# Kernel tuning notes

Hardware: AMD Instinct MI355X
Metric: run time of the kernel (lower is better)

The kernel has to match this reference:

```python
import jax, jax.numpy as jnp
import numpy as np

B, N, D, H = 4, 2048, 512, 8
HD = D // H  # 64


def setup_inputs() -> dict:
    key = jax.random.key(0)
    ks = jax.random.split(key, 12)
    s = 0.02
    return {
        "x": jax.random.normal(ks[0], (B, N, D), jnp.float32),
        "freqs": jax.random.normal(ks[1], (B, N, HD // 2), jnp.float32),
        # weights stored as (in, out); torch Linear applies x @ W.T + b
        "wqkv_w": jax.random.normal(ks[2], (D, 3 * D), jnp.float32) * s,
        "wqkv_b": jax.random.normal(ks[3], (3 * D,), jnp.float32) * s,
        "out_w": jax.random.normal(ks[4], (D, D), jnp.float32) * s,
        "out_b": jax.random.normal(ks[5], (D,), jnp.float32) * s,
        "ffn1_w": jax.random.normal(ks[6], (2 * D, 2 * D), jnp.float32) * s,
        "ffn1_b": jax.random.normal(ks[7], (2 * D,), jnp.float32) * s,
        "ln_g": jnp.ones((2 * D,), jnp.float32),
        "ln_b": jnp.zeros((2 * D,), jnp.float32),
        "ffn2_w": jax.random.normal(ks[8], (2 * D, D), jnp.float32) * s,
        "ffn2_b": jax.random.normal(ks[9], (D,), jnp.float32) * s,
    }


def _rope(t, cos, sin):
    # t: [B,H,N,HD]; cos/sin: [B,1,N,HD/2]
    x1, x2 = t[..., ::2], t[..., 1::2]
    return jnp.stack([x1 * cos - x2 * sin, x1 * sin + x2 * cos], axis=-1).reshape(t.shape)


def reference(x, freqs, wqkv_w, wqkv_b, out_w, out_b,
              ffn1_w, ffn1_b, ln_g, ln_b, ffn2_w, ffn2_b):
    b, n, d = x.shape
    h, hd = H, d // H
    qkv = x @ wqkv_w + wqkv_b                      # [B,N,3D]
    q, k, v = jnp.split(qkv, 3, axis=-1)
    to_heads = lambda t: t.reshape(b, n, h, hd).transpose(0, 2, 1, 3)  # [B,H,N,HD]
    q, k, v = to_heads(q), to_heads(k), to_heads(v)
    cos = jnp.cos(freqs)[:, None]                  # [B,1,N,HD/2]
    sin = jnp.sin(freqs)[:, None]
    q = _rope(q, cos, sin)
    k = _rope(k, cos, sin)
    scale = hd ** -0.5
    attn = jax.nn.softmax(jnp.einsum('bhqd,bhkd->bhqk', q, k) * scale, axis=-1)
    msg = jnp.einsum('bhqk,bhkd->bhqd', attn, v).transpose(0, 2, 1, 3).reshape(b, n, d)
    msg = msg @ out_w + out_b
    # FFN on concat([x, msg]): Linear -> LayerNorm -> GELU(exact) -> Linear
    hcat = jnp.concatenate([x, msg], axis=-1) @ ffn1_w + ffn1_b   # [B,N,2D]
    mu = hcat.mean(-1, keepdims=True)
    var = hcat.var(-1, keepdims=True)
    hcat = (hcat - mu) * jax.lax.rsqrt(var + 1e-5) * ln_g + ln_b
    hcat = jax.nn.gelu(hcat, approximate=False)
    return x + hcat @ ffn2_w + ffn2_b
```

## Files before the change

### kernel.cpp

```cpp
#include <hip/hip_runtime.h>
#include <hip/hip_bf16.h>
#include <math.h>

typedef __bf16 bf16;
typedef __bf16 bf16x2 __attribute__((ext_vector_type(2)));
typedef __bf16 bf16x4 __attribute__((ext_vector_type(4)));
typedef __bf16 bf16x8 __attribute__((ext_vector_type(8)));
typedef float f32x4 __attribute__((ext_vector_type(4)));
typedef float f32x16 __attribute__((ext_vector_type(16)));

#define MFMA16(a, b, c) __builtin_amdgcn_mfma_f32_16x16x32_bf16(a, b, c, 0, 0, 0)
#define MFMA32(a, b, c) __builtin_amdgcn_mfma_f32_32x32x16_bf16(a, b, c, 0, 0, 0)

#define GLD_LDS16(gp, lp)                                                          \
    __builtin_amdgcn_global_load_lds(                                              \
        (const __attribute__((address_space(1))) void*)(gp),                       \
        (__attribute__((address_space(3))) void*)(lp), 16, 0, 0)


__global__ __launch_bounds__(256) void transpose_all_kernel(
    const float* __restrict__ w0, const float* __restrict__ w1,
    const float* __restrict__ w2, const float* __restrict__ w3,
    bf16* __restrict__ d0, bf16* __restrict__ d1,
    bf16* __restrict__ d2, bf16* __restrict__ d3)
{
    const int bid = blockIdx.x;
    const float* src; bf16* dst; int R, C, bx, by;
    if (bid < 768)       { src = w0; dst = d0; R = 512;  C = 1536; int r = bid;        bx = r % 48; by = r / 48; }
    else if (bid < 1024) { src = w1; dst = d1; R = 512;  C = 512;  int r = bid - 768;  bx = r % 16; by = r / 16; }
    else if (bid < 2048) { src = w2; dst = d2; R = 1024; C = 1024; int r = bid - 1024; bx = r % 32; by = r / 32; }
    else                 { src = w3; dst = d3; R = 1024; C = 512;  int r = bid - 2048; bx = r % 16; by = r / 16; }
    __shared__ bf16 tile[32][33];
    const int tx = threadIdx.x & 31, ty = threadIdx.x >> 5;
    const int x = bx * 32 + tx;
#pragma unroll
    for (int j = 0; j < 4; j++)
        tile[ty + 8 * j][tx] = (bf16)src[(size_t)(by * 32 + ty + 8 * j) * C + x];
    __syncthreads();
    const int x2 = by * 32 + tx;
#pragma unroll
    for (int j = 0; j < 4; j++)
        dst[(size_t)(bx * 32 + ty + 8 * j) * R + x2] = tile[tx][ty + 8 * j];
}

__global__ __launch_bounds__(256) void cast_x_kernel(const float* __restrict__ x,
                                                     bf16* __restrict__ cat)
{
    int i = blockIdx.x * 256 + threadIdx.x;
    int row = i >> 7, col = (i & 127) << 2;
    const float4 v = *(const float4*)(&x[(size_t)row * 512 + col]);
    bf16x4 o; o[0] = (bf16)v.x; o[1] = (bf16)v.y; o[2] = (bf16)v.z; o[3] = (bf16)v.w;
    *(bf16x4*)(&cat[(size_t)row * 1024 + col]) = o;
}

__global__ __launch_bounds__(256) void rope_kernel(bf16* __restrict__ qb,
                                                   bf16* __restrict__ kb,
                                                   const float* __restrict__ freqs)
{
    const float SC = 0.125f * 1.44269504089f;
    const int bh = blockIdx.x >> 6, nblk = blockIdx.x & 63;
    const int g = threadIdx.x & 7, nl = threadIdx.x >> 3;
    const int n = nblk * 32 + nl;
    const int b = bh >> 3;
    const float4 f = *(const float4*)(&freqs[((size_t)b * 2048 + n) * 32 + g * 4]);
    const float cs[4] = {cosf(f.x), cosf(f.y), cosf(f.z), cosf(f.w)};
    const float sn[4] = {sinf(f.x), sinf(f.y), sinf(f.z), sinf(f.w)};
    const size_t off = ((size_t)bh * 2048 + n) * 64 + g * 8;
    bf16x8 q8 = *(bf16x8*)(qb + off);
    bf16x8 k8 = *(bf16x8*)(kb + off);
#pragma unroll
    for (int i = 0; i < 4; i++) {
        float q1 = q8[2 * i], q2 = q8[2 * i + 1];
        q8[2 * i]     = (bf16)((q1 * cs[i] - q2 * sn[i]) * SC);
        q8[2 * i + 1] = (bf16)((q1 * sn[i] + q2 * cs[i]) * SC);
        float k1 = k8[2 * i], k2 = k8[2 * i + 1];
        k8[2 * i]     = (bf16)(k1 * cs[i] - k2 * sn[i]);
        k8[2 * i + 1] = (bf16)(k1 * sn[i] + k2 * cs[i]);
    }
    *(bf16x8*)(qb + off) = q8;
    *(bf16x8*)(kb + off) = k8;
}

template <int MODE>
__global__ __launch_bounds__(256) void gemm_mfma(
    const bf16* __restrict__ A, int lda, const bf16* __restrict__ Bt,
    const float* __restrict__ bias, void* __restrict__ outv,
    const float* __restrict__ auxf, bf16* __restrict__ o1, bf16* __restrict__ o2,
    int K)
{
    const int tid = threadIdx.x;
    const int lane = tid & 63;
    const int wave = tid >> 6;
    const int wm = wave >> 1, wn = wave & 1;
    const int l15 = lane & 15, quad = lane >> 4;
    const int m0 = blockIdx.y * 128;
    const int n0 = blockIdx.x * 128;

    __shared__ bf16 As[128 * 32];
    __shared__ bf16 Bs[128 * 32];

    const int c0 = tid, c1 = tid + 256;
    const int r0 = c0 >> 2, kc0 = (c0 & 3) << 3;
    const int r1 = c1 >> 2, kc1 = (c1 & 3) << 3;

    const f32x4 zero = {0.f, 0.f, 0.f, 0.f};
    f32x4 acc[4][4];
#pragma unroll
    for (int i = 0; i < 4; i++)
#pragma unroll
        for (int j = 0; j < 4; j++) acc[i][j] = zero;

    for (int k0 = 0; k0 < K; k0 += 32) {
        GLD_LDS16(&A[(size_t)(m0 + r0) * lda + k0 + kc0], &As[c0 * 8]);
        GLD_LDS16(&A[(size_t)(m0 + r1) * lda + k0 + kc1], &As[c1 * 8]);
        GLD_LDS16(&Bt[(size_t)(n0 + r0) * K + k0 + kc0], &Bs[c0 * 8]);
        GLD_LDS16(&Bt[(size_t)(n0 + r1) * K + k0 + kc1], &Bs[c1 * 8]);
        __syncthreads();
        bf16x8 af[4], bfv[4];
#pragma unroll
        for (int t = 0; t < 4; t++) {
            af[t]  = *(const bf16x8*)(&As[(wm * 64 + t * 16 + l15) * 32 + quad * 8]);
            bfv[t] = *(const bf16x8*)(&Bs[(wn * 64 + t * 16 + l15) * 32 + quad * 8]);
        }
#pragma unroll
        for (int mt = 0; mt < 4; mt++)
#pragma unroll
            for (int nt = 0; nt < 4; nt++)
                acc[mt][nt] = MFMA16(af[mt], bfv[nt], acc[mt][nt]);
        __syncthreads();
    }

    const int row_base = m0 + wm * 64;
    const int col_base = n0 + wn * 64;

    if constexpr (MODE == 0) {
        const int sector = col_base >> 9;
        bf16* dstbase = (sector == 0) ? (bf16*)outv : (sector == 1 ? o1 : o2);
#pragma unroll
        for (int nt = 0; nt < 4; nt++) {
            const int col = col_base + nt * 16 + l15;
            const int cq = col & 511;
            const int h = cq >> 6, hd = cq & 63;
            const float bv = bias[col];
#pragma unroll
            for (int mt = 0; mt < 4; mt++) {
#pragma unroll
                for (int r = 0; r < 4; r++) {
                    const int mrow = row_base + mt * 16 + quad * 4 + r;
                    const int b = mrow >> 11, n = mrow & 2047;
                    dstbase[(((size_t)b * 8 + h) * 2048 + n) * 64 + hd] =
                        (bf16)(acc[mt][nt][r] + bv);
                }
            }
        }
    } else {
#pragma unroll
        for (int nt = 0; nt < 4; nt++) {
            const int col = col_base + nt * 16 + l15;
            const float bv = bias[col];
#pragma unroll
            for (int mt = 0; mt < 4; mt++) {
#pragma unroll
                for (int r = 0; r < 4; r++) {
                    const int row = row_base + mt * 16 + quad * 4 + r;
                    float v = acc[mt][nt][r] + bv;
                    if constexpr (MODE == 1) {
                        ((bf16*)outv)[(size_t)row * 1024 + 512 + col] = (bf16)v;
                    } else if constexpr (MODE == 2) {
                        ((bf16*)outv)[(size_t)row * 1024 + col] = (bf16)v;
                    } else {
                        v += auxf[(size_t)row * 512 + col];
                        ((float*)outv)[(size_t)row * 512 + col] = v;
                    }
                }
            }
        }
    }
}

__global__ __launch_bounds__(256) void attn_kernel(const bf16* __restrict__ qb,
                                                   const bf16* __restrict__ kb,
                                                   const bf16* __restrict__ vb,
                                                   bf16* __restrict__ ao)
{
    __shared__ bf16 Ks[128 * 72];
    __shared__ bf16 Vts[64 * 136];
    __shared__ bf16 Ps[4][32 * 72];

    const int tid = threadIdx.x, lane = tid & 63, wave = tid >> 6;
    const int l31 = lane & 31, half = lane >> 5;
    const int bh = blockIdx.x >> 4, qt = blockIdx.x & 15;
    const int b = bh >> 3, h = bh & 7;
    const size_t base = (size_t)bh * 2048 * 64;
    const int m0 = qt * 128 + wave * 32;

    bf16x8 aq[4];
#pragma unroll
    for (int k4 = 0; k4 < 4; k4++)
        aq[k4] = *(const bf16x8*)(&qb[base + (size_t)(m0 + l31) * 64 + k4 * 16 + half * 8]);

    f32x16 accO[2];
    float lsum[16];
#pragma unroll
    for (int i = 0; i < 16; i++) { accO[0][i] = 0.f; accO[1][i] = 0.f; lsum[i] = 0.f; }

    int krow[4], kcol[4], vpr[2], vdg[2];
#pragma unroll
    for (int i = 0; i < 4; i++) { int c = tid + i * 256; krow[i] = c >> 3; kcol[i] = (c & 7) << 3; }
#pragma unroll
    for (int i = 0; i < 2; i++) { int t = tid + i * 256; vpr[i] = t & 63; vdg[i] = t >> 6; }

    bf16x8 kreg[4], vreg0[2], vreg1[2];
    auto prefetch = [&](int key0) {
#pragma unroll
        for (int i = 0; i < 4; i++)
            kreg[i] = *(const bf16x8*)(&kb[base + (size_t)(key0 + krow[i]) * 64 + kcol[i]]);
#pragma unroll
        for (int i = 0; i < 2; i++) {
            vreg0[i] = *(const bf16x8*)(&vb[base + (size_t)(key0 + 2 * vpr[i]) * 64 + vdg[i] * 8]);
            vreg1[i] = *(const bf16x8*)(&vb[base + (size_t)(key0 + 2 * vpr[i] + 1) * 64 + vdg[i] * 8]);
        }
    };

    prefetch(0);
    for (int kt = 0; kt < 16; kt++) {
        __syncthreads();
#pragma unroll
        for (int i = 0; i < 4; i++)
            *(bf16x8*)(&Ks[krow[i] * 72 + kcol[i]]) = kreg[i];
#pragma unroll
        for (int i = 0; i < 2; i++) {
#pragma unroll
            for (int j = 0; j < 8; j++) {
                bf16x2 pr; pr[0] = vreg0[i][j]; pr[1] = vreg1[i][j];
                *(bf16x2*)(&Vts[(vdg[i] * 8 + j) * 136 + 2 * vpr[i]]) = pr;
            }
        }
        __syncthreads();
        if (kt < 15) prefetch((kt + 1) * 128);

#pragma unroll
        for (int sub = 0; sub < 2; sub++) {
            const int ko = sub * 64;
#pragma unroll
            for (int nb = 0; nb < 2; nb++) {
                f32x16 s;
#pragma unroll
                for (int i = 0; i < 16; i++) s[i] = 0.f;
#pragma unroll
                for (int k4 = 0; k4 < 4; k4++) {
                    bf16x8 bk = *(const bf16x8*)(&Ks[(ko + nb * 32 + l31) * 72 + k4 * 16 + half * 8]);
                    s = MFMA32(aq[k4], bk, s);
                }
#pragma unroll
                for (int r = 0; r < 16; r++) {
                    float pv = exp2f(s[r]);
                    lsum[r] += pv;
                    const int rowq = (r & 3) + 8 * (r >> 2) + 4 * half;
                    Ps[wave][rowq * 72 + nb * 32 + l31] = (bf16)pv;
                }
            }
#pragma unroll
            for (int kh = 0; kh < 4; kh++) {
                bf16x8 ap = *(const bf16x8*)(&Ps[wave][l31 * 72 + kh * 16 + half * 8]);
#pragma unroll
                for (int nb2 = 0; nb2 < 2; nb2++) {
                    bf16x8 bv = *(const bf16x8*)(&Vts[(nb2 * 32 + l31) * 136 + ko + kh * 16 + half * 8]);
                    accO[nb2] = MFMA32(ap, bv, accO[nb2]);
                }
            }
        }
    }

    float inv[16];
#pragma unroll
    for (int r = 0; r < 16; r++) {
        float s = lsum[r];
        s += __shfl_xor(s, 1); s += __shfl_xor(s, 2);
        s += __shfl_xor(s, 4); s += __shfl_xor(s, 8); s += __shfl_xor(s, 16);
        inv[r] = 1.0f / s;
    }

#pragma unroll
    for (int nb = 0; nb < 2; nb++) {
#pragma unroll
        for (int r = 0; r < 16; r++) {
            const int n = m0 + (r & 3) + 8 * (r >> 2) + 4 * half;
            ao[((size_t)b * 2048 + n) * 512 + h * 64 + nb * 32 + l31] =
                (bf16)(accO[nb][r] * inv[r]);
        }
    }
}

__global__ __launch_bounds__(256) void ln_gelu_kernel(bf16* __restrict__ hb,
                                                      const float* __restrict__ g,
                                                      const float* __restrict__ bt)
{
    const int row = blockIdx.x, tid = threadIdx.x;
    const int lane = tid & 63, wave = tid >> 6;
    bf16* hr = hb + (size_t)row * 1024;
    bf16x4 hv = *(const bf16x4*)(&hr[tid * 4]);
    float v0 = hv[0], v1 = hv[1], v2 = hv[2], v3 = hv[3];
    float s = v0 + v1 + v2 + v3;
    float q = v0 * v0 + v1 * v1 + v2 * v2 + v3 * v3;
    for (int o = 32; o; o >>= 1) { s += __shfl_xor(s, o); q += __shfl_xor(q, o); }
    __shared__ float red[8];
    if (lane == 0) { red[wave] = s; red[4 + wave] = q; }
    __syncthreads();
    s = red[0] + red[1] + red[2] + red[3];
    q = red[4] + red[5] + red[6] + red[7];
    const float mu = s * (1.f / 1024.f);
    const float rstd = rsqrtf(q * (1.f / 1024.f) - mu * mu + 1e-5f);
    const float4 gv = *(const float4*)(&g[tid * 4]);
    const float4 bv = *(const float4*)(&bt[tid * 4]);
    float vv[4] = {v0, v1, v2, v3};
    const float gg[4] = {gv.x, gv.y, gv.z, gv.w};
    const float bb[4] = {bv.x, bv.y, bv.z, bv.w};
    bf16x4 o4;
#pragma unroll
    for (int i = 0; i < 4; i++) {
        float y = (vv[i] - mu) * rstd * gg[i] + bb[i];
        float ge = 0.5f * y * (1.0f + erff(y * 0.70710678118f));
        o4[i] = (bf16)ge;
    }
    *(bf16x4*)(&hr[tid * 4]) = o4;
}

extern "C" void kernel_launch(void* const* d_in, const int* in_sizes, int n_in,
                              void* d_out, int out_size, void* d_ws, size_t ws_size,
                              hipStream_t stream) {
    (void)in_sizes; (void)n_in; (void)out_size; (void)ws_size;
    const float* x      = (const float*)d_in[0];
    const float* freqs  = (const float*)d_in[1];
    const float* wqkv_w = (const float*)d_in[2];
    const float* wqkv_b = (const float*)d_in[3];
    const float* out_w  = (const float*)d_in[4];
    const float* out_b  = (const float*)d_in[5];
    const float* ffn1_w = (const float*)d_in[6];
    const float* ffn1_b = (const float*)d_in[7];
    const float* ln_g   = (const float*)d_in[8];
    const float* ln_b   = (const float*)d_in[9];
    const float* ffn2_w = (const float*)d_in[10];
    const float* ffn2_b = (const float*)d_in[11];
    float* out = (float*)d_out;
    bf16* ws   = (bf16*)d_ws;

    bf16* wqkv_t = ws;
    bf16* out_t  = wqkv_t + 1536 * 512;
    bf16* ffn1_t = out_t + 512 * 512;
    bf16* ffn2_t = ffn1_t + 1024 * 1024;
    bf16* cat    = ffn2_t + 512 * 1024;
    bf16* qbuf   = cat + (size_t)8192 * 1024;
    bf16* kbuf   = qbuf + (size_t)8192 * 512;
    bf16* vbuf   = kbuf + (size_t)8192 * 512;
    bf16* aobuf  = vbuf + (size_t)8192 * 512;
    bf16* hbuf   = qbuf;

    transpose_all_kernel<<<2560, 256, 0, stream>>>(wqkv_w, out_w, ffn1_w, ffn2_w,
                                                   wqkv_t, out_t, ffn1_t, ffn2_t);
    cast_x_kernel<<<4096, 256, 0, stream>>>(x, cat);

    gemm_mfma<0><<<dim3(12, 64), 256, 0, stream>>>(cat, 1024, wqkv_t, wqkv_b, qbuf, nullptr, kbuf, vbuf, 512);
    rope_kernel<<<2048, 256, 0, stream>>>(qbuf, kbuf, freqs);
    attn_kernel<<<512, 256, 0, stream>>>(qbuf, kbuf, vbuf, aobuf);
    gemm_mfma<1><<<dim3(4, 64), 256, 0, stream>>>(aobuf, 512, out_t, out_b, cat, nullptr, nullptr, nullptr, 512);
    gemm_mfma<2><<<dim3(8, 64), 256, 0, stream>>>(cat, 1024, ffn1_t, ffn1_b, hbuf, nullptr, nullptr, nullptr, 1024);
    ln_gelu_kernel<<<8192, 256, 0, stream>>>(hbuf, ln_g, ln_b);
    gemm_mfma<3><<<dim3(4, 64), 256, 0, stream>>>(hbuf, 1024, ffn2_t, ffn2_b, out, x, nullptr, nullptr, 1024);
}
```

Measured before the change: 293.5 us.

## Keep attention probabilities in registers via transposed MFMA and register-prefetch GEMM tiles

The attention kernel now computes the transposed score tile (K as the A operand, Q as the B operand), so each lane holds one query row's probabilities. Those are packed to bf16 and swapped across wave halves with shuffles to form the PV MFMA operand directly, removing the per-wave LDS staging buffer and its store/load round trip. This also simplifies row-sum reduction and allows vectorized output stores. Separately, the GEMM replaces direct global-to-LDS loads with a register prefetch of the next K-slice that overlaps the MFMA work, at the cost of extra VGPRs and explicit LDS writes.

```diff
diff --git a/kernel.cpp b/kernel.cpp
--- a/kernel.cpp
+++ b/kernel.cpp
@@ -11,11 +11,6 @@
 
 #define MFMA16(a, b, c) __builtin_amdgcn_mfma_f32_16x16x32_bf16(a, b, c, 0, 0, 0)
 #define MFMA32(a, b, c) __builtin_amdgcn_mfma_f32_32x32x16_bf16(a, b, c, 0, 0, 0)
-
-#define GLD_LDS16(gp, lp)                                                          \
-    __builtin_amdgcn_global_load_lds(                                              \
-        (const __attribute__((address_space(1))) void*)(gp),                       \
-        (__attribute__((address_space(3))) void*)(lp), 16, 0, 0)
 
 
 __global__ __launch_bounds__(256) void transpose_all_kernel(
@@ -103,6 +98,11 @@
     const int r0 = c0 >> 2, kc0 = (c0 & 3) << 3;
     const int r1 = c1 >> 2, kc1 = (c1 & 3) << 3;
 
+    const bf16* pA0 = &A[(size_t)(m0 + r0) * lda + kc0];
+    const bf16* pA1 = &A[(size_t)(m0 + r1) * lda + kc1];
+    const bf16* pB0 = &Bt[(size_t)(n0 + r0) * K + kc0];
+    const bf16* pB1 = &Bt[(size_t)(n0 + r1) * K + kc1];
+
     const f32x4 zero = {0.f, 0.f, 0.f, 0.f};
     f32x4 acc[4][4];
 #pragma unroll
@@ -110,12 +110,24 @@
 #pragma unroll
         for (int j = 0; j < 4; j++) acc[i][j] = zero;
 
+    bf16x8 ra0 = *(const bf16x8*)pA0;
+    bf16x8 ra1 = *(const bf16x8*)pA1;
+    bf16x8 rb0 = *(const bf16x8*)pB0;
+    bf16x8 rb1 = *(const bf16x8*)pB1;
+
     for (int k0 = 0; k0 < K; k0 += 32) {
-        GLD_LDS16(&A[(size_t)(m0 + r0) * lda + k0 + kc0], &As[c0 * 8]);
-        GLD_LDS16(&A[(size_t)(m0 + r1) * lda + k0 + kc1], &As[c1 * 8]);
-        GLD_LDS16(&Bt[(size_t)(n0 + r0) * K + k0 + kc0], &Bs[c0 * 8]);
-        GLD_LDS16(&Bt[(size_t)(n0 + r1) * K + k0 + kc1], &Bs[c1 * 8]);
         __syncthreads();
+        *(bf16x8*)(&As[c0 * 8]) = ra0;
+        *(bf16x8*)(&As[c1 * 8]) = ra1;
+        *(bf16x8*)(&Bs[c0 * 8]) = rb0;
+        *(bf16x8*)(&Bs[c1 * 8]) = rb1;
+        __syncthreads();
+        if (k0 + 32 < K) {
+            ra0 = *(const bf16x8*)(pA0 + k0 + 32);
+            ra1 = *(const bf16x8*)(pA1 + k0 + 32);
+            rb0 = *(const bf16x8*)(pB0 + k0 + 32);
+            rb1 = *(const bf16x8*)(pB1 + k0 + 32);
+        }
         bf16x8 af[4], bfv[4];
 #pragma unroll
         for (int t = 0; t < 4; t++) {
@@ -127,7 +139,6 @@
 #pragma unroll
             for (int nt = 0; nt < 4; nt++)
                 acc[mt][nt] = MFMA16(af[mt], bfv[nt], acc[mt][nt]);
-        __syncthreads();
     }
 
     const int row_base = m0 + wm * 64;
@@ -185,7 +196,6 @@
 {
     __shared__ bf16 Ks[128 * 72];
     __shared__ bf16 Vts[64 * 136];
-    __shared__ bf16 Ps[4][32 * 72];
 
     const int tid = threadIdx.x, lane = tid & 63, wave = tid >> 6;
     const int l31 = lane & 31, half = lane >> 5;
@@ -200,9 +210,9 @@
         aq[k4] = *(const bf16x8*)(&qb[base + (size_t)(m0 + l31) * 64 + k4 * 16 + half * 8]);
 
     f32x16 accO[2];
-    float lsum[16];
-#pragma unroll
-    for (int i = 0; i < 16; i++) { accO[0][i] = 0.f; accO[1][i] = 0.f; lsum[i] = 0.f; }
+#pragma unroll
+    for (int i = 0; i < 16; i++) { accO[0][i] = 0.f; accO[1][i] = 0.f; }
+    float lsum = 0.f;
 
     int krow[4], kcol[4], vpr[2], vdg[2];
 #pragma unroll
@@ -240,54 +250,68 @@
         if (kt < 15) prefetch((kt + 1) * 128);
 
 #pragma unroll
-        for (int sub = 0; sub < 2; sub++) {
-            const int ko = sub * 64;
-#pragma unroll
-            for (int nb = 0; nb < 2; nb++) {
-                f32x16 s;
-#pragma unroll
-                for (int i = 0; i < 16; i++) s[i] = 0.f;
-#pragma unroll
-                for (int k4 = 0; k4 < 4; k4++) {
-                    bf16x8 bk = *(const bf16x8*)(&Ks[(ko + nb * 32 + l31) * 72 + k4 * 16 + half * 8]);
-                    s = MFMA32(aq[k4], bk, s);
-                }
-#pragma unroll
-                for (int r = 0; r < 16; r++) {
-                    float pv = exp2f(s[r]);
-                    lsum[r] += pv;
-                    const int rowq = (r & 3) + 8 * (r >> 2) + 4 * half;
-                    Ps[wave][rowq * 72 + nb * 32 + l31] = (bf16)pv;
-                }
-            }
-#pragma unroll
-            for (int kh = 0; kh < 4; kh++) {
-                bf16x8 ap = *(const bf16x8*)(&Ps[wave][l31 * 72 + kh * 16 + half * 8]);
-#pragma unroll
-                for (int nb2 = 0; nb2 < 2; nb2++) {
-                    bf16x8 bv = *(const bf16x8*)(&Vts[(nb2 * 32 + l31) * 136 + ko + kh * 16 + half * 8]);
-                    accO[nb2] = MFMA32(ap, bv, accO[nb2]);
-                }
-            }
-        }
-    }
-
-    float inv[16];
-#pragma unroll
-    for (int r = 0; r < 16; r++) {
-        float s = lsum[r];
-        s += __shfl_xor(s, 1); s += __shfl_xor(s, 2);
-        s += __shfl_xor(s, 4); s += __shfl_xor(s, 8); s += __shfl_xor(s, 16);
-        inv[r] = 1.0f / s;
-    }
-
-#pragma unroll
-    for (int nb = 0; nb < 2; nb++) {
-#pragma unroll
-        for (int r = 0; r < 16; r++) {
-            const int n = m0 + (r & 3) + 8 * (r >> 2) + 4 * half;
-            ao[((size_t)b * 2048 + n) * 512 + h * 64 + nb * 32 + l31] =
-                (bf16)(accO[nb][r] * inv[r]);
+        for (int nb = 0; nb < 4; nb++) {
+            const int ko = nb * 32;
+            f32x16 s;
+#pragma unroll
+            for (int i = 0; i < 16; i++) s[i] = 0.f;
+#pragma unroll
+            for (int k4 = 0; k4 < 4; k4++) {
+                bf16x8 ak = *(const bf16x8*)(&Ks[(ko + l31) * 72 + k4 * 16 + half * 8]);
+                s = MFMA32(ak, aq[k4], s);
+            }
+            float p[16];
+#pragma unroll
+            for (int r = 0; r < 16; r++) p[r] = exp2f(s[r]);
+            lsum += (((p[0] + p[1]) + (p[2] + p[3])) + ((p[4] + p[5]) + (p[6] + p[7])))
+                  + (((p[8] + p[9]) + (p[10] + p[11])) + ((p[12] + p[13]) + (p[14] + p[15])));
+            unsigned pk[8];
+#pragma unroll
+            for (int i2 = 0; i2 < 8; i2++) {
+                union { bf16x2 hh; unsigned u; } t;
+                t.hh[0] = (bf16)p[2 * i2]; t.hh[1] = (bf16)p[2 * i2 + 1];
+                pk[i2] = t.u;
+            }
+            const unsigned sa = half ? pk[0] : pk[2];
+            const unsigned sb = half ? pk[1] : pk[3];
+            const unsigned sc2 = half ? pk[4] : pk[6];
+            const unsigned sd = half ? pk[5] : pk[7];
+            const unsigned ra = (unsigned)__shfl_xor((int)sa, 32);
+            const unsigned rb = (unsigned)__shfl_xor((int)sb, 32);
+            const unsigned rc = (unsigned)__shfl_xor((int)sc2, 32);
+            const unsigned rd = (unsigned)__shfl_xor((int)sd, 32);
+            union { bf16x8 v; unsigned u[4]; } B0, B1;
+            B0.u[0] = half ? ra : pk[0];
+            B0.u[1] = half ? rb : pk[1];
+            B0.u[2] = half ? pk[2] : ra;
+            B0.u[3] = half ? pk[3] : rb;
+            B1.u[0] = half ? rc : pk[4];
+            B1.u[1] = half ? rd : pk[5];
+            B1.u[2] = half ? pk[6] : rc;
+            B1.u[3] = half ? pk[7] : rd;
+#pragma unroll
+            for (int dh = 0; dh < 2; dh++) {
+                bf16x8 av0 = *(const bf16x8*)(&Vts[(dh * 32 + l31) * 136 + ko + half * 8]);
+                bf16x8 av1 = *(const bf16x8*)(&Vts[(dh * 32 + l31) * 136 + ko + 16 + half * 8]);
+                accO[dh] = MFMA32(av0, B0.v, accO[dh]);
+                accO[dh] = MFMA32(av1, B1.v, accO[dh]);
+            }
+        }
+    }
+
+    lsum += __shfl_xor(lsum, 32);
+    const float inv = 1.0f / lsum;
+
+    const int n = m0 + l31;
+    bf16* aor = ao + ((size_t)b * 2048 + n) * 512 + h * 64;
+#pragma unroll
+    for (int dh = 0; dh < 2; dh++) {
+#pragma unroll
+        for (int g = 0; g < 4; g++) {
+            bf16x4 o4;
+#pragma unroll
+            for (int e = 0; e < 4; e++) o4[e] = (bf16)(accO[dh][g * 4 + e] * inv);
+            *(bf16x4*)(&aor[dh * 32 + g * 8 + half * 4]) = o4;
         }
     }
 }
```

Result: faster. 266.3 us (-9.3%).
